# Optimization experiments

Measured on AMD Instinct MI355X. Metric: run time of the kernel, lower is better.

The kernel has to match this reference:

```python
import jax, jax.numpy as jnp
import numpy as np

B, N, D, H, DM = 4, 1024, 1024, 16, 4096
DH = D // H
SCALE = DH ** -0.5
EPS = 1e-5


def layer_norm(x, g, b):
    mu = jnp.mean(x, axis=-1, keepdims=True)
    var = jnp.mean((x - mu) ** 2, axis=-1, keepdims=True)
    return (x - mu) * jax.lax.rsqrt(var + EPS) * g + b


def mha(q_in, k_in, v_in, Wq, bq, Wk, bk, Wv, bv, Wp, bp):
    # weights stored (in, out); torch Linear equivalent y = x @ W + b
    q = (q_in @ Wq + bq).reshape(B, -1, H, DH).transpose(0, 2, 1, 3)  # (B,H,Nq,DH)
    k = (k_in @ Wk + bk).reshape(B, -1, H, DH).transpose(0, 2, 1, 3)
    v = (v_in @ Wv + bv).reshape(B, -1, H, DH).transpose(0, 2, 1, 3)
    attn = jax.nn.softmax(jnp.einsum('bhqd,bhkd->bhqk', q, k) * SCALE, axis=-1)
    x = jnp.einsum('bhqk,bhkd->bhqd', attn, v).transpose(0, 2, 1, 3).reshape(B, -1, D)
    return x @ Wp + bp


def setup_inputs() -> dict:
    key = jax.random.key(0)
    ks = jax.random.split(key, 32)
    s = 0.02
    inp = {
        'tokens_enc': jax.random.normal(ks[0], (B, N, D), jnp.float32),
        'tokens_dec': jax.random.normal(ks[1], (B, N, D), jnp.float32),
        'PE_enc': jax.random.normal(ks[2], (B, N, D), jnp.float32),
        'PE_dec': jax.random.normal(ks[3], (B, N, D), jnp.float32),
    }
    names = ['sa_Wq', 'sa_Wk', 'sa_Wv', 'sa_Wp', 'ca_Wq', 'ca_Wk', 'ca_Wv', 'ca_Wp']
    for i, n in enumerate(names):
        inp[n] = jax.random.normal(ks[4 + i], (D, D), jnp.float32) * s
        inp[n.replace('W', 'b')] = jnp.zeros((D,), jnp.float32)
    inp['mlp_W1'] = jax.random.normal(ks[12], (D, DM), jnp.float32) * s
    inp['mlp_b1'] = jnp.zeros((DM,), jnp.float32)
    inp['mlp_W2'] = jax.random.normal(ks[13], (DM, D), jnp.float32) * s
    inp['mlp_b2'] = jnp.zeros((D,), jnp.float32)
    for i in (1, 2, 3):
        inp[f'ln{i}_g'] = jnp.ones((D,), jnp.float32)
        inp[f'ln{i}_b'] = jnp.zeros((D,), jnp.float32)
    return inp


def reference(tokens_enc, tokens_dec, PE_enc, PE_dec,
              sa_Wq, sa_bq, sa_Wk, sa_bk, sa_Wv, sa_bv, sa_Wp, sa_bp,
              ca_Wq, ca_bq, ca_Wk, ca_bk, ca_Wv, ca_bv, ca_Wp, ca_bp,
              mlp_W1, mlp_b1, mlp_W2, mlp_b2,
              ln1_g, ln1_b, ln2_g, ln2_b, ln3_g, ln3_b):
    # SA (pre-norm): q=k=ln(x)+PE_dec, v=ln(x)
    x2 = layer_norm(tokens_dec, ln1_g, ln1_b)
    qk = x2 + PE_dec
    tokens_dec = tokens_dec + mha(qk, qk, x2, sa_Wq, sa_bq, sa_Wk, sa_bk, sa_Wv, sa_bv, sa_Wp, sa_bp)
    # CA: q=ln(x)+PE_dec, k=enc+PE_enc, v=enc
    x2 = layer_norm(tokens_dec, ln2_g, ln2_b)
    tokens_dec = tokens_dec + mha(x2 + PE_dec, tokens_enc + PE_enc, tokens_enc,
                                  ca_Wq, ca_bq, ca_Wk, ca_bk, ca_Wv, ca_bv, ca_Wp, ca_bp)
    # FFD
    x2 = layer_norm(tokens_dec, ln3_g, ln3_b)
    h = jax.nn.gelu(x2 @ mlp_W1 + mlp_b1, approximate=False)
    return tokens_dec + (h @ mlp_W2 + mlp_b2)
```

## Files before the change

### kernel.cpp

```cpp
#include <hip/hip_runtime.h>
#include <hip/hip_bf16.h>
#include <math.h>

#define B_ 4
#define N_ 1024
#define D_ 1024
#define H_ 16
#define DH_ 64
#define DM_ 4096
#define NT_ (B_*N_)
#define EPS_ 1e-5f
#define SCALE_ 0.125f
#define CEXP_ 0.1803368801111244f

typedef unsigned short u16;
typedef short s16x8 __attribute__((ext_vector_type(8)));
typedef __bf16 y16x8 __attribute__((ext_vector_type(8)));
typedef float f32x4 __attribute__((ext_vector_type(4)));
typedef float f32x16 __attribute__((ext_vector_type(16)));

#define ZERO16 (f32x16){0.f,0.f,0.f,0.f,0.f,0.f,0.f,0.f,0.f,0.f,0.f,0.f,0.f,0.f,0.f,0.f}

__device__ __forceinline__ u16 f2bs(float f) {
  unsigned int u = __builtin_bit_cast(unsigned int, f);
  u += 0x7fffu + ((u >> 16) & 1u);
  return (u16)(u >> 16);
}

static __device__ __forceinline__ f32x4 MFMA(y16x8 a, y16x8 b, f32x4 c) {
  return __builtin_amdgcn_mfma_f32_16x16x32_bf16(a, b, c, 0, 0, 0);
}
static __device__ __forceinline__ f32x16 MFMA32(y16x8 a, y16x8 b, f32x16 c) {
  return __builtin_amdgcn_mfma_f32_32x32x16_bf16(a, b, c, 0, 0, 0);
}

static __device__ __forceinline__ unsigned cvtpk(float a, float b) {
  unsigned r;
  asm("v_cvt_pk_bf16_f32 %0, %1, %2" : "=v"(r) : "v"(a), "v"(b));
  return r;
}

static __device__ __forceinline__ void async16(void* lds, const void* g) {
  __builtin_amdgcn_global_load_lds(
      (const __attribute__((address_space(1))) unsigned int*)g,
      (__attribute__((address_space(3))) unsigned int*)lds, 16, 0, 0);
}

__global__ __launch_bounds__(256) void k_wtrans8(
    const float* __restrict__ s0, const float* __restrict__ s1,
    const float* __restrict__ s2, const float* __restrict__ s3,
    const float* __restrict__ s4, const float* __restrict__ s5,
    const float* __restrict__ s6, const float* __restrict__ s7,
    u16* __restrict__ dst) {
  const float* W = blockIdx.z == 0 ? s0 : blockIdx.z == 1 ? s1 : blockIdx.z == 2 ? s2
                 : blockIdx.z == 3 ? s3 : blockIdx.z == 4 ? s4 : blockIdx.z == 5 ? s5
                 : blockIdx.z == 6 ? s6 : s7;
  u16* Wt = dst + (size_t)blockIdx.z * D_ * D_;
  __shared__ u16 tile[32][33];
  int n0 = blockIdx.x * 32, k0 = blockIdx.y * 32;
  int tx = threadIdx.x & 31, ty = threadIdx.x >> 5;
#pragma unroll
  for (int i = 0; i < 4; ++i) {
    int k = k0 + ty + i * 8;
    tile[ty + i * 8][tx] = f2bs(W[(size_t)k * D_ + n0 + tx]);
  }
  __syncthreads();
#pragma unroll
  for (int i = 0; i < 4; ++i) {
    int n = n0 + ty + i * 8;
    Wt[(size_t)n * D_ + k0 + tx] = tile[tx][ty + i * 8];
  }
}

__global__ __launch_bounds__(256) void k_wtrans(const float* __restrict__ W,
                                                u16* __restrict__ Wt,
                                                int K, int Ncols) {
  __shared__ u16 tile[32][33];
  int n0 = blockIdx.x * 32, k0 = blockIdx.y * 32;
  int tx = threadIdx.x & 31, ty = threadIdx.x >> 5;
#pragma unroll
  for (int i = 0; i < 4; ++i) {
    int k = k0 + ty + i * 8;
    tile[ty + i * 8][tx] = f2bs(W[(size_t)k * Ncols + n0 + tx]);
  }
  __syncthreads();
#pragma unroll
  for (int i = 0; i < 4; ++i) {
    int n = n0 + ty + i * 8;
    Wt[(size_t)n * K + k0 + tx] = tile[tx][ty + i * 8];
  }
}

__global__ __launch_bounds__(256) void k_encprep(const float* __restrict__ enc,
                                                 const float* __restrict__ pe,
                                                 u16* __restrict__ encpe,
                                                 u16* __restrict__ encv) {
  int i = blockIdx.x * 256 + threadIdx.x;
  float4 e = ((const float4*)enc)[i];
  float4 p = ((const float4*)pe)[i];
  union { u16 u[4]; uint2 v; } a, b;
  a.u[0] = f2bs(e.x + p.x); a.u[1] = f2bs(e.y + p.y);
  a.u[2] = f2bs(e.z + p.z); a.u[3] = f2bs(e.w + p.w);
  b.u[0] = f2bs(e.x); b.u[1] = f2bs(e.y); b.u[2] = f2bs(e.z); b.u[3] = f2bs(e.w);
  ((uint2*)encpe)[i] = a.v;
  ((uint2*)encv)[i] = b.v;
}

__global__ __launch_bounds__(256) void k_ln(const float* __restrict__ x,
                                            const float* __restrict__ g,
                                            const float* __restrict__ bta,
                                            const float* __restrict__ pe,
                                            u16* __restrict__ x2o,
                                            u16* __restrict__ qko) {
  int row = blockIdx.x;
  int t = threadIdx.x;
  float4 v = ((const float4*)(x + (size_t)row * D_))[t];
  float s = v.x + v.y + v.z + v.w;
#pragma unroll
  for (int o = 1; o < 64; o <<= 1) s += __shfl_xor(s, o, 64);
  __shared__ float red[8];
  if ((t & 63) == 0) red[t >> 6] = s;
  __syncthreads();
  float mean = (red[0] + red[1] + red[2] + red[3]) * (1.0f / D_);
  float dx = v.x - mean, dy = v.y - mean, dz = v.z - mean, dw = v.w - mean;
  float s2 = dx * dx + dy * dy + dz * dz + dw * dw;
#pragma unroll
  for (int o = 1; o < 64; o <<= 1) s2 += __shfl_xor(s2, o, 64);
  if ((t & 63) == 0) red[4 + (t >> 6)] = s2;
  __syncthreads();
  float var = (red[4] + red[5] + red[6] + red[7]) * (1.0f / D_);
  float rstd = rsqrtf(var + EPS_);
  float4 gv = ((const float4*)g)[t];
  float4 bv = ((const float4*)bta)[t];
  float y0 = dx * rstd * gv.x + bv.x;
  float y1 = dy * rstd * gv.y + bv.y;
  float y2 = dz * rstd * gv.z + bv.z;
  float y3 = dw * rstd * gv.w + bv.w;
  union { u16 u[4]; uint2 v2; } o1;
  o1.u[0] = f2bs(y0); o1.u[1] = f2bs(y1); o1.u[2] = f2bs(y2); o1.u[3] = f2bs(y3);
  ((uint2*)(x2o + (size_t)row * D_))[t] = o1.v2;
  if (pe) {
    float4 pv = ((const float4*)(pe + (size_t)row * D_))[t];
    union { u16 u[4]; uint2 v2; } o2;
    o2.u[0] = f2bs(y0 + pv.x); o2.u[1] = f2bs(y1 + pv.y);
    o2.u[2] = f2bs(y2 + pv.z); o2.u[3] = f2bs(y3 + pv.w);
    ((uint2*)(qko + (size_t)row * D_))[t] = o2.v2;
  }
}

template <int EPI, int BN>
__global__ __launch_bounds__(256) void k_gemm2(const u16* __restrict__ A,
                                               const u16* __restrict__ Bt,
                                               const float* __restrict__ bias,
                                               const float* __restrict__ res,
                                               float* __restrict__ outf,
                                               u16* __restrict__ outb,
                                               int M, int Nn, int K, int ldo) {
  constexpr int BM = 128, BK = 64;
  constexpr int FN = BN / 32;
  __shared__ __align__(128) char smem[(BM + BN) * BK * 2];
  const int t = threadIdx.x;
  const int wave = t >> 6, lane = t & 63, lg = lane >> 4, lc = lane & 15;
  const int nwg = gridDim.x * gridDim.y;
  const int bid = blockIdx.y * gridDim.x + blockIdx.x;
  const int lb = (bid & 7) * (nwg >> 3) + (bid >> 3);
  const int bx = lb % gridDim.x, by = lb / gridDim.x;
  const int m0 = by * BM, n0 = bx * BN;
  const int wm = (wave >> 1) * 64, wn = (wave & 1) * (BN / 2);
  f32x4 acc[4][FN];
#pragma unroll
  for (int i = 0; i < 4; ++i)
#pragma unroll
    for (int j = 0; j < FN; ++j) acc[i][j] = (f32x4){0.f, 0.f, 0.f, 0.f};
  const char* Ag = (const char*)(A + (size_t)m0 * K);
  const char* Bg = (const char*)(Bt + (size_t)n0 * K);
  char* sA = smem;
  char* sB = smem + BM * BK * 2;
  const int sr = t >> 3, sp = t & 7;

  for (int kt = 0; kt < K; kt += BK) {
    __syncthreads();
#pragma unroll
    for (int rr = 0; rr < 4; ++rr) {
      int row = rr * 32 + sr;
      int c = sp ^ (row & 7);
      async16(sA + (size_t)row * 128 + sp * 16,
              Ag + ((size_t)row * K + kt + c * 8) * 2);
    }
#pragma unroll
    for (int rr = 0; rr < BN / 32; ++rr) {
      int row = rr * 32 + sr;
      int c = sp ^ (row & 7);
      async16(sB + (size_t)row * 128 + sp * 16,
              Bg + ((size_t)row * K + kt + c * 8) * 2);
    }
    __syncthreads();
#pragma unroll
    for (int ks = 0; ks < 2; ++ks) {
      y16x8 af[4], bfr[FN];
#pragma unroll
      for (int fm = 0; fm < 4; ++fm) {
        int R = wm + fm * 16 + lc;
        int pc = (ks * 4 + lg) ^ (R & 7);
        af[fm] = *(const y16x8*)(sA + (size_t)R * 128 + pc * 16);
      }
#pragma unroll
      for (int fn = 0; fn < FN; ++fn) {
        int R = wn + fn * 16 + lc;
        int pc = (ks * 4 + lg) ^ (R & 7);
        bfr[fn] = *(const y16x8*)(sB + (size_t)R * 128 + pc * 16);
      }
#pragma unroll
      for (int fm = 0; fm < 4; ++fm)
#pragma unroll
        for (int fn = 0; fn < FN; ++fn)
          acc[fm][fn] = MFMA(af[fm], bfr[fn], acc[fm][fn]);
    }
  }

#pragma unroll
  for (int fm = 0; fm < 4; ++fm)
#pragma unroll
    for (int fn = 0; fn < FN; ++fn)
#pragma unroll
      for (int j = 0; j < 4; ++j) {
        int row = m0 + wm + fm * 16 + lg * 4 + j;
        int col = n0 + wn + fn * 16 + lc;
        float vv = acc[fm][fn][j] + bias[col];
        size_t idx = (size_t)row * ldo + col;
        if constexpr (EPI == 0) {
          outb[idx] = f2bs(vv);
        } else if constexpr (EPI == 1) {
          outf[idx] = vv + res[idx];
        } else {
          float gx = 0.5f * vv * (1.0f + erff(vv * 0.70710678118f));
          outb[idx] = f2bs(gx);
        }
      }
}

__global__ __launch_bounds__(512) void k_gemmG(
    const u16* __restrict__ A0, const u16* __restrict__ A1,
    const u16* __restrict__ A2, const u16* __restrict__ A3,
    const u16* __restrict__ A4, const u16* __restrict__ W0,
    const u16* __restrict__ W1, const u16* __restrict__ W2,
    const u16* __restrict__ W3, const u16* __restrict__ W4,
    const float* __restrict__ b0, const float* __restrict__ b1,
    const float* __restrict__ b2, const float* __restrict__ b3,
    const float* __restrict__ b4, u16* __restrict__ qk1,
    u16* __restrict__ vt1, u16* __restrict__ qk2, u16* __restrict__ vt2) {
  constexpr int BM = 128, BN = 128, BK = 64, K = D_;
  __shared__ __align__(128) char smem[2][(BM + BN) * BK * 2];
  const int z = blockIdx.z;
  const u16* A = z == 0 ? A0 : z == 1 ? A1 : z == 2 ? A2 : z == 3 ? A3 : A4;
  const u16* Bt = z == 0 ? W0 : z == 1 ? W1 : z == 2 ? W2 : z == 3 ? W3 : W4;
  const float* bias = z == 0 ? b0 : z == 1 ? b1 : z == 2 ? b2 : z == 3 ? b3 : b4;
  const int t = threadIdx.x;
  const int wave = t >> 6, lane = t & 63, lg = lane >> 4, lc = lane & 15;
  const int nwg = gridDim.x * gridDim.y;
  const int bid = blockIdx.y * gridDim.x + blockIdx.x;
  const int lb = (bid & 7) * (nwg >> 3) + (bid >> 3);
  const int bx = lb % gridDim.x, by = lb / gridDim.x;
  const int m0 = by * BM, n0 = bx * BN;
  const int wm = (wave >> 2) * 64, wn = (wave & 3) * 32;
  f32x4 acc[4][2];
#pragma unroll
  for (int i = 0; i < 4; ++i)
#pragma unroll
    for (int j = 0; j < 2; ++j) acc[i][j] = (f32x4){0.f, 0.f, 0.f, 0.f};
  const char* Ag = (const char*)(A + (size_t)m0 * K);
  const char* Bg = (const char*)(Bt + (size_t)n0 * K);
  const int sr = t >> 3, sp = t & 7;

  auto stage = [&](int bufi, int kt) {
    char* sA = smem[bufi];
    char* sB = smem[bufi] + BM * BK * 2;
#pragma unroll
    for (int rr = 0; rr < 2; ++rr) {
      int row = rr * 64 + sr;
      int c = sp ^ (row & 7);
      async16(sA + (size_t)row * 128 + sp * 16,
              Ag + ((size_t)row * K + kt + c * 8) * 2);
      async16(sB + (size_t)row * 128 + sp * 16,
              Bg + ((size_t)row * K + kt + c * 8) * 2);
    }
  };
  auto compute = [&](int bufi) {
    const char* sA = smem[bufi];
    const char* sB = smem[bufi] + BM * BK * 2;
#pragma unroll
    for (int ks = 0; ks < 2; ++ks) {
      y16x8 af[4], bfr[2];
#pragma unroll
      for (int fm = 0; fm < 4; ++fm) {
        int R = wm + fm * 16 + lc;
        int pc = (ks * 4 + lg) ^ (R & 7);
        af[fm] = *(const y16x8*)(sA + (size_t)R * 128 + pc * 16);
      }
#pragma unroll
      for (int fn = 0; fn < 2; ++fn) {
        int R = wn + fn * 16 + lc;
        int pc = (ks * 4 + lg) ^ (R & 7);
        bfr[fn] = *(const y16x8*)(sB + (size_t)R * 128 + pc * 16);
      }
#pragma unroll
      for (int fm = 0; fm < 4; ++fm)
#pragma unroll
        for (int fn = 0; fn < 2; ++fn)
          acc[fm][fn] = MFMA(af[fm], bfr[fn], acc[fm][fn]);
    }
  };

  stage(0, 0);
  __syncthreads();
  int cur = 0;
  for (int kt = BK; kt < K; kt += BK) {
    stage(cur ^ 1, kt);
    compute(cur);
    __syncthreads();
    cur ^= 1;
  }
  compute(cur);

  const bool isV = (z == 2) || (z == 4);
  if (!isV) {
    u16* outqk = (z == 3) ? qk2 : qk1;
    const int coff = (z == 1 || z == 3) ? D_ : 0;
#pragma unroll
    for (int fm = 0; fm < 4; ++fm)
#pragma unroll
      for (int fn = 0; fn < 2; ++fn)
#pragma unroll
        for (int j = 0; j < 4; ++j) {
          int row = m0 + wm + fm * 16 + lg * 4 + j;
          int col = n0 + wn + fn * 16 + lc;
          outqk[(size_t)row * (2 * D_) + coff + col] =
              f2bs(acc[fm][fn][j] + bias[col]);
        }
  } else {
    u16* outvt = (z == 2) ? vt1 : vt2;
#pragma unroll
    for (int fm = 0; fm < 4; ++fm)
#pragma unroll
      for (int fn = 0; fn < 2; ++fn) {
        int row0 = m0 + wm + fm * 16 + lg * 4;
        int col = n0 + wn + fn * 16 + lc;
        int bb = row0 >> 10, nn = row0 & (N_ - 1);
        int h = col >> 6, dh = col & 63;
        float bcol = bias[col];
        union { u16 u[4]; uint2 v; } pk;
#pragma unroll
        for (int j = 0; j < 4; ++j) pk.u[j] = f2bs(acc[fm][fn][j] + bcol);
        *(uint2*)&outvt[(((size_t)bb * H_ + h) * DH_ + dh) * N_ + nn] = pk.v;
      }
  }
}

__global__ __launch_bounds__(256) void k_attn(const u16* __restrict__ q, int qs,
                                              const u16* __restrict__ k, int ks2,
                                              const u16* __restrict__ vt,
                                              u16* __restrict__ out) {
  __shared__ __align__(16) u16 Kl[64][64];
  __shared__ __align__(16) u16 Vl[64][64];
  __shared__ __align__(16) u16 Ol[4][32][72];
  const int lb = blockIdx.x;
  const int bh = (lb & 7) | ((lb >> 6) << 3);
  const int qb = (lb >> 3) & 7;
  const int b = bh >> 4, h = bh & 15;
  const int t = threadIdx.x, wave = t >> 6, lane = t & 63;
  const int ql = lane & 31, hi = lane >> 5;
  const int q0 = qb * 128 + wave * 32;
  const u16* qp = q + ((size_t)b * N_ + q0) * qs + h * DH_;
  const u16* kp = k + (size_t)b * N_ * ks2 + h * DH_;
  const u16* vp = vt + ((size_t)bh * DH_) * N_;

  y16x8 aq[4];
#pragma unroll
  for (int s = 0; s < 4; ++s)
    aq[s] = *(const y16x8*)(qp + (size_t)ql * qs + s * 16 + hi * 8);

  f32x16 o0 = ZERO16, o1 = ZERO16;
  float m_r = -1e30f, l_r = 0.f;

  for (int kt = 0; kt < N_; kt += 64) {
    __syncthreads();
#pragma unroll
    for (int rr = 0; rr < 2; ++rr) {
      int id = rr * 256 + t;
      int row = id >> 3, c = id & 7;
      int pc2 = c ^ (row & 7);
      *(s16x8*)&Kl[row][pc2 * 8] =
          *(const s16x8*)(kp + (size_t)(kt + row) * ks2 + c * 8);
      *(s16x8*)&Vl[row][pc2 * 8] =
          *(const s16x8*)(vp + (size_t)row * N_ + kt + c * 8);
    }
    __syncthreads();

    f32x16 st0 = ZERO16, st1 = ZERO16;
#pragma unroll
    for (int s = 0; s < 4; ++s) {
      int pc0 = ((s * 2 + hi) ^ (ql & 7)) * 8;
      y16x8 ak0 = *(const y16x8*)&Kl[ql][pc0];
      y16x8 ak1 = *(const y16x8*)&Kl[32 + ql][pc0];
      st0 = MFMA32(ak0, aq[s], st0);
      st1 = MFMA32(ak1, aq[s], st1);
    }

    float mx = st0[0];
#pragma unroll
    for (int r = 1; r < 16; ++r) mx = fmaxf(mx, st0[r]);
#pragma unroll
    for (int r = 0; r < 16; ++r) mx = fmaxf(mx, st1[r]);
    mx = fmaxf(mx, __shfl_xor(mx, 32, 64));
    float mn = fmaxf(m_r, mx);
    float corr = exp2f((m_r - mn) * CEXP_);
    float ps = 0.f;
#pragma unroll
    for (int r = 0; r < 16; ++r) {
      float e = exp2f((st0[r] - mn) * CEXP_); st0[r] = e; ps += e;
    }
#pragma unroll
    for (int r = 0; r < 16; ++r) {
      float e = exp2f((st1[r] - mn) * CEXP_); st1[r] = e; ps += e;
    }
    ps += __shfl_xor(ps, 32, 64);
    l_r = l_r * corr + ps;
    m_r = mn;
    o0 = o0 * corr;
    o1 = o1 * corr;

#pragma unroll
    for (int ks = 0; ks < 4; ++ks) {
      unsigned A0, A1, B0, B1;
      if (ks < 2) {
        const int il = ks * 8;
        A0 = cvtpk(st0[il + 0], st0[il + 1]);
        A1 = cvtpk(st0[il + 2], st0[il + 3]);
        B0 = cvtpk(st0[il + 4], st0[il + 5]);
        B1 = cvtpk(st0[il + 6], st0[il + 7]);
      } else {
        const int il = (ks - 2) * 8;
        A0 = cvtpk(st1[il + 0], st1[il + 1]);
        A1 = cvtpk(st1[il + 2], st1[il + 3]);
        B0 = cvtpk(st1[il + 4], st1[il + 5]);
        B1 = cvtpk(st1[il + 6], st1[il + 7]);
      }
      asm("v_permlane32_swap_b32 %0, %1" : "+v"(A0), "+v"(B0));
      asm("v_permlane32_swap_b32 %0, %1" : "+v"(A1), "+v"(B1));
      union { unsigned w[4]; y16x8 v; } fr;
      fr.w[0] = A0; fr.w[1] = A1; fr.w[2] = B0; fr.w[3] = B1;
      int pc = ((ks * 2 + hi) ^ (ql & 7)) * 8;
      y16x8 bv0 = *(const y16x8*)&Vl[ql][pc];
      y16x8 bv1 = *(const y16x8*)&Vl[32 + ql][pc];
      o0 = MFMA32(bv0, fr.v, o0);
      o1 = MFMA32(bv1, fr.v, o1);
    }
  }

  float rl = 1.f / l_r;
#pragma unroll
  for (int rq = 0; rq < 4; ++rq)
#pragma unroll
    for (int e = 0; e < 4; e += 2) {
      *(unsigned*)&Ol[wave][ql][8 * rq + 4 * hi + e] =
          cvtpk(o0[rq * 4 + e] * rl, o0[rq * 4 + e + 1] * rl);
      *(unsigned*)&Ol[wave][ql][32 + 8 * rq + 4 * hi + e] =
          cvtpk(o1[rq * 4 + e] * rl, o1[rq * 4 + e + 1] * rl);
    }
#pragma unroll
  for (int pp = 0; pp < 4; ++pp) {
    int row = pp * 8 + (lane >> 3);
    s16x8 vv = *(const s16x8*)&Ol[wave][row][(lane & 7) * 8];
    *(s16x8*)(out + ((size_t)b * N_ + q0 + row) * D_ + h * DH_ + (lane & 7) * 8) = vv;
  }
}

extern "C" void kernel_launch(void* const* d_in, const int* in_sizes, int n_in,
                              void* d_out, int out_size, void* d_ws, size_t ws_size,
                              hipStream_t stream) {
  const float* tokens_enc = (const float*)d_in[0];
  const float* tokens_dec = (const float*)d_in[1];
  const float* PE_enc = (const float*)d_in[2];
  const float* PE_dec = (const float*)d_in[3];
  const float* sa_Wq = (const float*)d_in[4];  const float* sa_bq = (const float*)d_in[5];
  const float* sa_Wk = (const float*)d_in[6];  const float* sa_bk = (const float*)d_in[7];
  const float* sa_Wv = (const float*)d_in[8];  const float* sa_bv = (const float*)d_in[9];
  const float* sa_Wp = (const float*)d_in[10]; const float* sa_bp = (const float*)d_in[11];
  const float* ca_Wq = (const float*)d_in[12]; const float* ca_bq = (const float*)d_in[13];
  const float* ca_Wk = (const float*)d_in[14]; const float* ca_bk = (const float*)d_in[15];
  const float* ca_Wv = (const float*)d_in[16]; const float* ca_bv = (const float*)d_in[17];
  const float* ca_Wp = (const float*)d_in[18]; const float* ca_bp = (const float*)d_in[19];
  const float* mlp_W1 = (const float*)d_in[20]; const float* mlp_b1 = (const float*)d_in[21];
  const float* mlp_W2 = (const float*)d_in[22]; const float* mlp_b2 = (const float*)d_in[23];
  const float* ln1_g = (const float*)d_in[24]; const float* ln1_b = (const float*)d_in[25];
  const float* ln2_g = (const float*)d_in[26]; const float* ln2_b = (const float*)d_in[27];
  const float* ln3_g = (const float*)d_in[28]; const float* ln3_b = (const float*)d_in[29];

  char* wsp = (char*)d_ws;
  size_t off = 0;
  auto alloc = [&](size_t bytes) -> char* {
    char* p = wsp + off;
    off += (bytes + 255) & ~(size_t)255;
    return p;
  };
  u16* w8   = (u16*)alloc((size_t)8 * D_ * D_ * 2);
  u16* w1T  = (u16*)alloc((size_t)DM_ * D_ * 2);
  u16* w2T  = (u16*)alloc((size_t)D_ * DM_ * 2);
  u16* encpe = (u16*)alloc((size_t)NT_ * D_ * 2);
  u16* encv  = (u16*)alloc((size_t)NT_ * D_ * 2);
  u16* x2b = (u16*)alloc((size_t)NT_ * D_ * 2);
  u16* qkb = (u16*)alloc((size_t)NT_ * D_ * 2);
  u16* qkm = (u16*)alloc((size_t)NT_ * 2 * D_ * 2);
  u16* qkm2 = (u16*)alloc((size_t)NT_ * 2 * D_ * 2);
  u16* vtb = (u16*)alloc((size_t)NT_ * D_ * 2);
  u16* vtb2 = (u16*)alloc((size_t)NT_ * D_ * 2);
  u16* attb = (u16*)alloc((size_t)NT_ * D_ * 2);
  float* dec1 = (float*)alloc((size_t)NT_ * D_ * 4);
  float* dec2 = (float*)alloc((size_t)NT_ * D_ * 4);
  u16* hb = (u16*)alloc((size_t)NT_ * DM_ * 2);

  const size_t DD = (size_t)D_ * D_;
  u16* wqT  = w8;
  u16* wkT  = w8 + 1 * DD;
  u16* wvT  = w8 + 2 * DD;
  u16* wpT  = w8 + 3 * DD;
  u16* cwqT = w8 + 4 * DD;
  u16* cwkT = w8 + 5 * DD;
  u16* cwvT = w8 + 6 * DD;
  u16* cwpT = w8 + 7 * DD;

  k_wtrans8<<<dim3(32, 32, 8), 256, 0, stream>>>(sa_Wq, sa_Wk, sa_Wv, sa_Wp,
                                                 ca_Wq, ca_Wk, ca_Wv, ca_Wp, w8);
  k_wtrans<<<dim3(128, 32), 256, 0, stream>>>(mlp_W1, w1T, D_, DM_);
  k_wtrans<<<dim3(32, 128), 256, 0, stream>>>(mlp_W2, w2T, DM_, D_);
  k_encprep<<<dim3(NT_ * D_ / 1024), 256, 0, stream>>>(tokens_enc, PE_enc, encpe, encv);

  k_ln<<<dim3(NT_), 256, 0, stream>>>(tokens_dec, ln1_g, ln1_b, PE_dec, x2b, qkb);
  k_gemmG<<<dim3(8, 32, 5), 512, 0, stream>>>(
      qkb, qkb, x2b, encpe, encv, wqT, wkT, wvT, cwkT, cwvT,
      sa_bq, sa_bk, sa_bv, ca_bk, ca_bv, qkm, vtb, qkm2, vtb2);
  k_attn<<<dim3(512), 256, 0, stream>>>(qkm, 2 * D_, qkm + D_, 2 * D_, vtb, attb);
  k_gemm2<1, 64><<<dim3(16, 32), 256, 0, stream>>>(attb, wpT, sa_bp, tokens_dec,
                                                   dec1, nullptr, NT_, D_, D_, D_);

  k_ln<<<dim3(NT_), 256, 0, stream>>>(dec1, ln2_g, ln2_b, PE_dec, x2b, qkb);
  k_gemm2<0, 64><<<dim3(16, 32), 256, 0, stream>>>(qkb, cwqT, ca_bq, nullptr,
                                                   nullptr, qkm2, NT_, D_, D_, 2 * D_);
  k_attn<<<dim3(512), 256, 0, stream>>>(qkm2, 2 * D_, qkm2 + D_, 2 * D_, vtb2, attb);
  k_gemm2<1, 64><<<dim3(16, 32), 256, 0, stream>>>(attb, cwpT, ca_bp, dec1,
                                                   dec2, nullptr, NT_, D_, D_, D_);

  k_ln<<<dim3(NT_), 256, 0, stream>>>(dec2, ln3_g, ln3_b, nullptr, x2b, nullptr);
  k_gemm2<2, 128><<<dim3(32, 32), 256, 0, stream>>>(x2b, w1T, mlp_b1, nullptr,
                                                    nullptr, hb, NT_, DM_, D_, DM_);
  k_gemm2<1, 64><<<dim3(16, 32), 256, 0, stream>>>(hb, w2T, mlp_b2, dec2,
                                                   (float*)d_out, nullptr, NT_, D_, DM_, D_);
}
```

Baseline: 386.5 us.

## Double-buffer LDS in GEMM kernel and switch to 512-thread 8-wave tiles

Replaces the single-buffered 256-thread GEMM with a 512-thread version whose shared-memory tiles are double-buffered. The next K-slice is issued asynchronously while the current one is computed, leaving one barrier per iteration. Tiles are now BM x 128 with 8 waves each owning a 32-column strip, and the launch grids are reshaped to match. Each wave gets fewer accumulators, and shared-memory use doubles, which may reduce occupancy.

After: 350.4 us. 1.1x faster.

```diff
diff --git a/kernel.cpp b/kernel.cpp
--- a/kernel.cpp
+++ b/kernel.cpp
@@ -148,17 +148,17 @@
   }
 }
 
-template <int EPI, int BN>
-__global__ __launch_bounds__(256) void k_gemm2(const u16* __restrict__ A,
-                                               const u16* __restrict__ Bt,
-                                               const float* __restrict__ bias,
-                                               const float* __restrict__ res,
-                                               float* __restrict__ outf,
-                                               u16* __restrict__ outb,
-                                               int M, int Nn, int K, int ldo) {
-  constexpr int BM = 128, BK = 64;
-  constexpr int FN = BN / 32;
-  __shared__ __align__(128) char smem[(BM + BN) * BK * 2];
+template <int EPI, int BM>
+__global__ __launch_bounds__(512) void k_gemm(const u16* __restrict__ A,
+                                              const u16* __restrict__ Bt,
+                                              const float* __restrict__ bias,
+                                              const float* __restrict__ res,
+                                              float* __restrict__ outf,
+                                              u16* __restrict__ outb,
+                                              int M, int Nn, int K, int ldo) {
+  constexpr int BN = 128, BK = 64;
+  constexpr int FM = BM / 32;
+  __shared__ __align__(128) char smem[2][(BM + BN) * BK * 2];
   const int t = threadIdx.x;
   const int wave = t >> 6, lane = t & 63, lg = lane >> 4, lc = lane & 15;
   const int nwg = gridDim.x * gridDim.y;
@@ -166,62 +166,75 @@
   const int lb = (bid & 7) * (nwg >> 3) + (bid >> 3);
   const int bx = lb % gridDim.x, by = lb / gridDim.x;
   const int m0 = by * BM, n0 = bx * BN;
-  const int wm = (wave >> 1) * 64, wn = (wave & 1) * (BN / 2);
-  f32x4 acc[4][FN];
-#pragma unroll
-  for (int i = 0; i < 4; ++i)
-#pragma unroll
-    for (int j = 0; j < FN; ++j) acc[i][j] = (f32x4){0.f, 0.f, 0.f, 0.f};
+  const int wm = (wave >> 2) * (BM / 2), wn = (wave & 3) * 32;
+  f32x4 acc[FM][2];
+#pragma unroll
+  for (int i = 0; i < FM; ++i)
+#pragma unroll
+    for (int j = 0; j < 2; ++j) acc[i][j] = (f32x4){0.f, 0.f, 0.f, 0.f};
   const char* Ag = (const char*)(A + (size_t)m0 * K);
   const char* Bg = (const char*)(Bt + (size_t)n0 * K);
-  char* sA = smem;
-  char* sB = smem + BM * BK * 2;
   const int sr = t >> 3, sp = t & 7;
 
-  for (int kt = 0; kt < K; kt += BK) {
-    __syncthreads();
-#pragma unroll
-    for (int rr = 0; rr < 4; ++rr) {
-      int row = rr * 32 + sr;
+  auto stage = [&](int bufi, int kt) {
+    char* sA = smem[bufi];
+    char* sB = smem[bufi] + BM * BK * 2;
+#pragma unroll
+    for (int rr = 0; rr < BM / 64; ++rr) {
+      int row = rr * 64 + sr;
       int c = sp ^ (row & 7);
       async16(sA + (size_t)row * 128 + sp * 16,
               Ag + ((size_t)row * K + kt + c * 8) * 2);
     }
 #pragma unroll
-    for (int rr = 0; rr < BN / 32; ++rr) {
-      int row = rr * 32 + sr;
+    for (int rr = 0; rr < 2; ++rr) {
+      int row = rr * 64 + sr;
       int c = sp ^ (row & 7);
       async16(sB + (size_t)row * 128 + sp * 16,
               Bg + ((size_t)row * K + kt + c * 8) * 2);
     }
-    __syncthreads();
+  };
+  auto compute = [&](int bufi) {
+    const char* sA = smem[bufi];
+    const char* sB = smem[bufi] + BM * BK * 2;
 #pragma unroll
     for (int ks = 0; ks < 2; ++ks) {
-      y16x8 af[4], bfr[FN];
-#pragma unroll
-      for (int fm = 0; fm < 4; ++fm) {
+      y16x8 af[FM], bfr[2];
+#pragma unroll
+      for (int fm = 0; fm < FM; ++fm) {
         int R = wm + fm * 16 + lc;
         int pc = (ks * 4 + lg) ^ (R & 7);
         af[fm] = *(const y16x8*)(sA + (size_t)R * 128 + pc * 16);
       }
 #pragma unroll
-      for (int fn = 0; fn < FN; ++fn) {
+      for (int fn = 0; fn < 2; ++fn) {
         int R = wn + fn * 16 + lc;
         int pc = (ks * 4 + lg) ^ (R & 7);
         bfr[fn] = *(const y16x8*)(sB + (size_t)R * 128 + pc * 16);
       }
 #pragma unroll
-      for (int fm = 0; fm < 4; ++fm)
-#pragma unroll
-        for (int fn = 0; fn < FN; ++fn)
+      for (int fm = 0; fm < FM; ++fm)
+#pragma unroll
+        for (int fn = 0; fn < 2; ++fn)
           acc[fm][fn] = MFMA(af[fm], bfr[fn], acc[fm][fn]);
     }
-  }
-
-#pragma unroll
-  for (int fm = 0; fm < 4; ++fm)
-#pragma unroll
-    for (int fn = 0; fn < FN; ++fn)
+  };
+
+  stage(0, 0);
+  __syncthreads();
+  int cur = 0;
+  for (int kt = BK; kt < K; kt += BK) {
+    stage(cur ^ 1, kt);
+    compute(cur);
+    __syncthreads();
+    cur ^= 1;
+  }
+  compute(cur);
+
+#pragma unroll
+  for (int fm = 0; fm < FM; ++fm)
+#pragma unroll
+    for (int fn = 0; fn < 2; ++fn)
 #pragma unroll
       for (int j = 0; j < 4; ++j) {
         int row = m0 + wm + fm * 16 + lg * 4 + j;
@@ -540,19 +553,19 @@
       qkb, qkb, x2b, encpe, encv, wqT, wkT, wvT, cwkT, cwvT,
       sa_bq, sa_bk, sa_bv, ca_bk, ca_bv, qkm, vtb, qkm2, vtb2);
   k_attn<<<dim3(512), 256, 0, stream>>>(qkm, 2 * D_, qkm + D_, 2 * D_, vtb, attb);
-  k_gemm2<1, 64><<<dim3(16, 32), 256, 0, stream>>>(attb, wpT, sa_bp, tokens_dec,
-                                                   dec1, nullptr, NT_, D_, D_, D_);
+  k_gemm<1, 64><<<dim3(8, 64), 512, 0, stream>>>(attb, wpT, sa_bp, tokens_dec,
+                                                 dec1, nullptr, NT_, D_, D_, D_);
 
   k_ln<<<dim3(NT_), 256, 0, stream>>>(dec1, ln2_g, ln2_b, PE_dec, x2b, qkb);
-  k_gemm2<0, 64><<<dim3(16, 32), 256, 0, stream>>>(qkb, cwqT, ca_bq, nullptr,
-                                                   nullptr, qkm2, NT_, D_, D_, 2 * D_);
+  k_gemm<0, 64><<<dim3(8, 64), 512, 0, stream>>>(qkb, cwqT, ca_bq, nullptr,
+                                                 nullptr, qkm2, NT_, D_, D_, 2 * D_);
   k_attn<<<dim3(512), 256, 0, stream>>>(qkm2, 2 * D_, qkm2 + D_, 2 * D_, vtb2, attb);
-  k_gemm2<1, 64><<<dim3(16, 32), 256, 0, stream>>>(attb, cwpT, ca_bp, dec1,
-                                                   dec2, nullptr, NT_, D_, D_, D_);
+  k_gemm<1, 64><<<dim3(8, 64), 512, 0, stream>>>(attb, cwpT, ca_bp, dec1,
+                                                 dec2, nullptr, NT_, D_, D_, D_);
 
   k_ln<<<dim3(NT_), 256, 0, stream>>>(dec2, ln3_g, ln3_b, nullptr, x2b, nullptr);
-  k_gemm2<2, 128><<<dim3(32, 32), 256, 0, stream>>>(x2b, w1T, mlp_b1, nullptr,
-                                                    nullptr, hb, NT_, DM_, D_, DM_);
-  k_gemm2<1, 64><<<dim3(16, 32), 256, 0, stream>>>(hb, w2T, mlp_b2, dec2,
-                                                   (float*)d_out, nullptr, NT_, D_, DM_, D_);
-}
+  k_gemm<2, 128><<<dim3(32, 32), 512, 0, stream>>>(x2b, w1T, mlp_b1, nullptr,
+                                                   nullptr, hb, NT_, DM_, D_, DM_);
+  k_gemm<1, 64><<<dim3(8, 64), 512, 0, stream>>>(hb, w2T, mlp_b2, dec2,
+                                                 (float*)d_out, nullptr, NT_, D_, DM_, D_);
+}
```
